# Kernel tuning notes

Hardware: AMD Instinct MI355X
Metric: run time of the kernel (lower is better)

## Reference

```python
import jax, jax.numpy as jnp
import numpy as np

NUM_HEADS = 16


def setup_inputs() -> dict:
    key = jax.random.key(0)
    k1, k2, k3 = jax.random.split(key, 3)
    S, B, E = 2048, 4, 1024
    std = float(np.sqrt(2.0 / (E + E)))
    query = jax.random.normal(k1, (S, B, E), dtype=jnp.float32)
    in_proj_weight = jax.random.normal(k2, (3 * E, E), dtype=jnp.float32) * std
    in_proj_bias = jnp.zeros((3 * E,), dtype=jnp.float32)
    out_proj_weight = jax.random.normal(k3, (E, E), dtype=jnp.float32) * std
    out_proj_bias = jnp.zeros((E,), dtype=jnp.float32)
    return {
        "query": query,
        "in_proj_weight": in_proj_weight,
        "in_proj_bias": in_proj_bias,
        "out_proj_weight": out_proj_weight,
        "out_proj_bias": out_proj_bias,
    }


def reference(query, in_proj_weight, in_proj_bias, out_proj_weight, out_proj_bias):
    S, B, E = query.shape
    H = NUM_HEADS
    hd = E // H
    scale = hd ** -0.5
    # fused QKV projection: [S, B, 3E]
    lin = jnp.einsum("sbe,fe->sbf", query, in_proj_weight) + in_proj_bias
    # torch layout: view(S, B*H, 3, hd) -> interleaved [h, {q,k,v}, hd]
    lin = lin.reshape(S, B * H, 3, hd)
    q = lin[:, :, 0, :]  # [S, B*H, hd]
    k = lin[:, :, 1, :]
    v = lin[:, :, 2, :]
    # scores: [B*H, S_q, S_k]
    scores = jnp.einsum("sbd,tbd->bst", q, k) * scale
    attn = jax.nn.softmax(scores.astype(jnp.float32), axis=-1).astype(scores.dtype)
    # context: [S, B*H, hd] -> [S, B, E]
    ctx = jnp.einsum("bst,tbd->sbd", attn, v).reshape(S, B, E)
    out = jnp.einsum("sbe,fe->sbf", ctx, out_proj_weight) + out_proj_bias
    return out
```

## Files before the change

### kernel.cpp

```cpp
#include <hip/hip_runtime.h>
#include <hip/hip_bf16.h>

typedef __hip_bfloat16 bf16;
typedef __attribute__((ext_vector_type(8))) short short8;
typedef __attribute__((ext_vector_type(4))) float floatx4;

#define GLD_LDS(g, l) __builtin_amdgcn_global_load_lds( \
    (const __attribute__((address_space(1))) void*)(g), \
    (__attribute__((address_space(3))) void*)(l), 16, 0, 0)

#define CS 0.18033688f

__global__ __launch_bounds__(256)
void cvt3_kernel(const float* __restrict__ q,  bf16* __restrict__ qo,
                 const float* __restrict__ w1, bf16* __restrict__ w1o,
                 const float* __restrict__ w2, bf16* __restrict__ w2o)
{
    const int i = blockIdx.x * 256 + threadIdx.x;
    const float* src; bf16* dst; long off;
    if (i < 1048576)       { src = q;  dst = qo;  off = (long)i * 8; }
    else if (i < 1441792)  { src = w1; dst = w1o; off = (long)(i - 1048576) * 8; }
    else                   { src = w2; dst = w2o; off = (long)(i - 1441792) * 8; }
    floatx4 a = *(const floatx4*)(src + off);
    floatx4 b = *(const floatx4*)(src + off + 4);
    short8 h;
    #pragma unroll
    for (int e = 0; e < 4; ++e) {
        union { bf16 v; short s; } u0, u1;
        u0.v = __float2bfloat16(a[e]); h[e]     = u0.s;
        u1.v = __float2bfloat16(b[e]); h[e + 4] = u1.s;
    }
    *(short8*)(dst + off) = h;
}

__device__ __forceinline__ void stage_f32(const float* __restrict__ src, int ld,
                                          bf16* lds, int t)
{
    const int sr = t >> 1;
    const int sc = (t & 1) * 16;
    const float* g = src + (long)sr * ld + sc;
    floatx4 f[4];
    #pragma unroll
    for (int i = 0; i < 4; ++i) f[i] = *(const floatx4*)(g + i * 4);
    short8 h[2];
    #pragma unroll
    for (int v = 0; v < 2; ++v)
        #pragma unroll
        for (int e = 0; e < 8; ++e) {
            union { bf16 b; short s; } u;
            u.b = __float2bfloat16(f[v * 2 + (e >> 2)][e & 3]);
            h[v][e] = u.s;
        }
    *(short8*)(lds + sr * 32 + sc)     = h[0];
    *(short8*)(lds + sr * 32 + sc + 8) = h[1];
}

template<int EPI, int AF32, int BF32>
__global__ __launch_bounds__(256, 2)
void gemm_bt(const void* __restrict__ Ap, const void* __restrict__ Bp,
             const float* __restrict__ bias,
             void* __restrict__ o0, bf16* __restrict__ o1, bf16* __restrict__ o2,
             int K, int N)
{
    __shared__ __align__(16) bf16 lA[128 * 32];
    __shared__ __align__(16) bf16 lB[128 * 32];

    const int t    = threadIdx.x;
    const int lane = t & 63;
    const int w    = t >> 6;
    const int mBase = blockIdx.y * 128;
    const int nBase = blockIdx.x * 128;
    const int wr = (w >> 1) * 64;
    const int wc = (w & 1) * 64;

    const int rowL = t >> 2;
    const int colL = (t & 3) * 8;
    const bf16* gA0 = (const bf16*)Ap + (long)(mBase + rowL) * K + colL;
    const bf16* gA1 = (const bf16*)Ap + (long)(mBase + rowL + 64) * K + colL;
    const bf16* gB0 = (const bf16*)Bp + (long)(nBase + rowL) * K + colL;
    const bf16* gB1 = (const bf16*)Bp + (long)(nBase + rowL + 64) * K + colL;
    char* lAb = (char*)lA + w * 1024;
    char* lBb = (char*)lB + w * 1024;

    floatx4 acc[4][4] = {};

    for (int k0 = 0; k0 < K; k0 += 32) {
        if constexpr (AF32) {
            stage_f32((const float*)Ap + (long)mBase * K + k0, K, lA, t);
        } else {
            GLD_LDS(gA0 + k0, lAb);
            GLD_LDS(gA1 + k0, lAb + 4096);
        }
        if constexpr (BF32) {
            stage_f32((const float*)Bp + (long)nBase * K + k0, K, lB, t);
        } else {
            GLD_LDS(gB0 + k0, lBb);
            GLD_LDS(gB1 + k0, lBb + 4096);
        }
        asm volatile("s_waitcnt vmcnt(0)" ::: "memory");
        __syncthreads();

        short8 af[4], bfr[4];
        #pragma unroll
        for (int m = 0; m < 4; ++m)
            af[m] = *(const short8*)(lA + (wr + m * 16 + (lane & 15)) * 32 + (lane >> 4) * 8);
        #pragma unroll
        for (int n = 0; n < 4; ++n)
            bfr[n] = *(const short8*)(lB + (wc + n * 16 + (lane & 15)) * 32 + (lane >> 4) * 8);
        #pragma unroll
        for (int m = 0; m < 4; ++m)
            #pragma unroll
            for (int n = 0; n < 4; ++n)
                acc[m][n] = __builtin_amdgcn_mfma_f32_16x16x32_bf16(af[m], bfr[n], acc[m][n], 0, 0, 0);
        __syncthreads();
    }

    #pragma unroll
    for (int m = 0; m < 4; ++m) {
        #pragma unroll
        for (int n = 0; n < 4; ++n) {
            const int col = nBase + wc + n * 16 + (lane & 15);
            const int r0  = mBase + wr + m * 16 + ((lane >> 4) << 2);
            const float bv = bias[col];
            if constexpr (EPI == 0) {
                const int h   = col / 192;
                const int rem = col % 192;
                const int qkv = rem >> 6;
                const int d   = rem & 63;
                #pragma unroll
                for (int j = 0; j < 4; ++j) {
                    const int r = r0 + j;
                    const int s = r >> 2;
                    const int b = r & 3;
                    const float v = acc[m][n][j] + bv;
                    if (qkv == 0)
                        ((bf16*)o0)[(((((b << 4) + h) << 11) + s) << 6) + d] =
                            __float2bfloat16(v * CS);
                    else if (qkv == 1)
                        o1[(((((b << 4) + h) << 11) + s) << 6) + d] = __float2bfloat16(v);
                    else
                        o2[((((b << 4) + h) << 17)) + (d << 11) + s] = __float2bfloat16(v);
                }
            } else {
                #pragma unroll
                for (int j = 0; j < 4; ++j)
                    ((float*)o0)[(long)(r0 + j) * N + col] = acc[m][n][j] + bv;
            }
        }
    }
}

__global__ __launch_bounds__(256, 2)
void attn_kernel(const bf16* __restrict__ Q, const bf16* __restrict__ Kg,
                 const bf16* __restrict__ Vt, bf16* __restrict__ Ctx)
{
    __shared__ __align__(16) bf16 lK[64 * 64];
    __shared__ __align__(16) bf16 lV[64 * 64];

    const int t    = threadIdx.x;
    const int lane = t & 63;
    const int w    = t >> 6;
    const int f    = lane & 15;
    const int g    = lane >> 4;
    const int bh   = blockIdx.y;
    const int q0   = blockIdx.x * 128 + w * 32;
    const long hb  = (long)bh * 2048 * 64;
    const bf16* Qh = Q  + hb;
    const bf16* Kh = Kg + hb;
    const bf16* Vh = Vt + hb;

    const int srow = t >> 3;
    const int scol = (t & 7) * 8;
    const int sig0 = (srow & 3) | ((srow & 16) >> 2) | ((srow & 12) << 1);
    const int wb0 = ((srow)      * 128 + scol * 2) ^ (((srow)      & 7) << 4);
    const int wb1 = ((srow + 32) * 128 + scol * 2) ^ (((srow + 32) & 7) << 4);

    short8 qf[2][2];
    #pragma unroll
    for (int m = 0; m < 2; ++m)
        #pragma unroll
        for (int kk = 0; kk < 2; ++kk)
            qf[m][kk] = *(const short8*)(Qh + (q0 + m * 16 + f) * 64 + kk * 32 + g * 8);

    floatx4 o[2][4] = {};
    float lrun[2] = {0.f, 0.f};
    const int srcBase = g * 20;

    short8 kR0 = *(const short8*)(Kh + (long)sig0 * 64 + scol);
    short8 kR1 = *(const short8*)(Kh + (long)(sig0 + 32) * 64 + scol);
    short8 vR0 = *(const short8*)(Vh + (long)srow * 2048 + scol);
    short8 vR1 = *(const short8*)(Vh + (long)(srow + 32) * 2048 + scol);

    for (int t0 = 0; t0 < 2048; t0 += 64) {
        *(short8*)((char*)lK + wb0) = kR0;
        *(short8*)((char*)lK + wb1) = kR1;
        *(short8*)((char*)lV + wb0) = vR0;
        *(short8*)((char*)lV + wb1) = vR1;
        __syncthreads();

        short8 kf[4][2];
        #pragma unroll
        for (int n = 0; n < 4; ++n)
            #pragma unroll
            for (int kk = 0; kk < 2; ++kk) {
                const int key = n * 16 + f;
                const int byte = (key * 128 + kk * 64 + g * 16) ^ ((key & 7) << 4);
                kf[n][kk] = *(const short8*)((char*)lK + byte);
            }

        if (t0 + 64 < 2048) {
            kR0 = *(const short8*)(Kh + (long)(t0 + 64 + sig0) * 64 + scol);
            kR1 = *(const short8*)(Kh + (long)(t0 + 64 + sig0 + 32) * 64 + scol);
            vR0 = *(const short8*)(Vh + (long)srow * 2048 + t0 + 64 + scol);
            vR1 = *(const short8*)(Vh + (long)(srow + 32) * 2048 + t0 + 64 + scol);
        }

        floatx4 sa2[4][2] = {};
        __builtin_amdgcn_s_setprio(1);
        #pragma unroll
        for (int n = 0; n < 4; ++n)
            #pragma unroll
            for (int m = 0; m < 2; ++m)
                #pragma unroll
                for (int kk = 0; kk < 2; ++kk)
                    sa2[n][m] = __builtin_amdgcn_mfma_f32_16x16x32_bf16(kf[n][kk], qf[m][kk], sa2[n][m], 0, 0, 0);
        __builtin_amdgcn_s_setprio(0);

        short8 vf[4][2];
        #pragma unroll
        for (int n2 = 0; n2 < 4; ++n2)
            #pragma unroll
            for (int kk = 0; kk < 2; ++kk) {
                const int dim = n2 * 16 + f;
                const int byte = (dim * 128 + kk * 64 + g * 16) ^ ((dim & 7) << 4);
                vf[n2][kk] = *(const short8*)((char*)lV + byte);
            }

        #pragma unroll
        for (int m = 0; m < 2; ++m)
            #pragma unroll
            for (int n = 0; n < 4; ++n)
                #pragma unroll
                for (int j = 0; j < 4; ++j) {
                    const float p = exp2f(sa2[n][m][j]);
                    sa2[n][m][j] = p;
                    lrun[m] += p;
                }

        short8 pf[2][2];
        #pragma unroll
        for (int m = 0; m < 2; ++m)
            #pragma unroll
            for (int kk = 0; kk < 2; ++kk)
                #pragma unroll
                for (int e = 0; e < 8; ++e) {
                    union { bf16 b; short s; } u;
                    u.b = __float2bfloat16(sa2[2 * kk + (e >> 2)][m][e & 3]);
                    pf[m][kk][e] = u.s;
                }

        __builtin_amdgcn_s_setprio(1);
        #pragma unroll
        for (int m = 0; m < 2; ++m)
            #pragma unroll
            for (int n2 = 0; n2 < 4; ++n2)
                #pragma unroll
                for (int kk = 0; kk < 2; ++kk)
                    o[m][n2] = __builtin_amdgcn_mfma_f32_16x16x32_bf16(pf[m][kk], vf[n2][kk], o[m][n2], 0, 0, 0);
        __builtin_amdgcn_s_setprio(0);

        __syncthreads();
    }

    const int b = bh >> 4;
    const int h = bh & 15;
    #pragma unroll
    for (int m = 0; m < 2; ++m) {
        lrun[m] += __shfl_xor(lrun[m], 16);
        lrun[m] += __shfl_xor(lrun[m], 32);
        float inv[4];
        #pragma unroll
        for (int j = 0; j < 4; ++j)
            inv[j] = 1.f / __shfl(lrun[m], srcBase + j);
        #pragma unroll
        for (int n2 = 0; n2 < 4; ++n2) {
            const int dim = (h << 6) + n2 * 16 + f;
            #pragma unroll
            for (int j = 0; j < 4; ++j) {
                const int srw = q0 + m * 16 + (g << 2) + j;
                Ctx[(((srw << 2) + b) << 10) + dim] = __float2bfloat16(o[m][n2][j] * inv[j]);
            }
        }
    }
}

extern "C" void kernel_launch(void* const* d_in, const int* in_sizes, int n_in,
                              void* d_out, int out_size, void* d_ws, size_t ws_size,
                              hipStream_t stream)
{
    const float* query = (const float*)d_in[0];
    const float* wIn   = (const float*)d_in[1];
    const float* bIn   = (const float*)d_in[2];
    const float* wOut  = (const float*)d_in[3];
    const float* bOut  = (const float*)d_in[4];

    const size_t HEADSZ = (size_t)64 * 2048 * 64;
    bf16* Qws = (bf16*)d_ws;
    bf16* Kws = Qws + HEADSZ;
    bf16* Vtw = Kws + HEADSZ;
    bf16* Ctx = Vtw + HEADSZ;
    bf16* qbf = Ctx;
    if (ws_size < 4 * HEADSZ * sizeof(bf16)) return;

    const size_t NEED_BIG = (4 * HEADSZ + 3145728 + 1048576) * sizeof(bf16);
    if (ws_size >= NEED_BIG) {
        bf16* wInBf  = Ctx + HEADSZ;
        bf16* wOutBf = wInBf + 3145728;
        cvt3_kernel<<<dim3(6144), 256, 0, stream>>>(query, qbf, wIn, wInBf, wOut, wOutBf);
        gemm_bt<0, 0, 0><<<dim3(24, 64), 256, 0, stream>>>(qbf, wInBf, bIn,
                                                           Qws, Kws, Vtw, 1024, 3072);
        attn_kernel<<<dim3(16, 64), 256, 0, stream>>>(Qws, Kws, Vtw, Ctx);
        gemm_bt<1, 0, 0><<<dim3(8, 64), 256, 0, stream>>>(Ctx, wOutBf, bOut,
                                                          d_out, nullptr, nullptr, 1024, 1024);
    } else {
        cvt3_kernel<<<dim3(4096), 256, 0, stream>>>(query, qbf, nullptr, nullptr, nullptr, nullptr);
        gemm_bt<0, 0, 1><<<dim3(24, 64), 256, 0, stream>>>(qbf, wIn, bIn,
                                                           Qws, Kws, Vtw, 1024, 3072);
        attn_kernel<<<dim3(16, 64), 256, 0, stream>>>(Qws, Kws, Vtw, Ctx);
        gemm_bt<1, 0, 1><<<dim3(8, 64), 256, 0, stream>>>(Ctx, wOut, bOut,
                                                          d_out, nullptr, nullptr, 1024, 1024);
    }
}
```

Measured before the change: 224.5 us.

## Double-buffer K/V tiles in LDS and compute softmax denominator via MFMA

Switches the attention kernel to double-buffered LDS for K and V, so the next tile is written into the alternate buffer while the current one is consumed, leaving one barrier per tile instead of two. The row-sum of exponentials is now computed by an extra MFMA against a vector of bf16 ones rather than by scalar adds and cross-lane shuffles. This sums the bf16-rounded probabilities, which matches what is fed to the P·V product. The cost is double the LDS footprint and extra MFMA work per tile.

```diff
diff --git a/kernel.cpp b/kernel.cpp
--- a/kernel.cpp
+++ b/kernel.cpp
@@ -154,8 +154,8 @@
 void attn_kernel(const bf16* __restrict__ Q, const bf16* __restrict__ Kg,
                  const bf16* __restrict__ Vt, bf16* __restrict__ Ctx)
 {
-    __shared__ __align__(16) bf16 lK[64 * 64];
-    __shared__ __align__(16) bf16 lV[64 * 64];
+    __shared__ __align__(16) bf16 lK[2][64 * 64];
+    __shared__ __align__(16) bf16 lV[2][64 * 64];
 
     const int t    = threadIdx.x;
     const int lane = t & 63;
@@ -182,22 +182,29 @@
         for (int kk = 0; kk < 2; ++kk)
             qf[m][kk] = *(const short8*)(Qh + (q0 + m * 16 + f) * 64 + kk * 32 + g * 8);
 
+    short8 ones;
+    #pragma unroll
+    for (int e = 0; e < 8; ++e) ones[e] = (short)0x3F80;
+
     floatx4 o[2][4] = {};
-    float lrun[2] = {0.f, 0.f};
-    const int srcBase = g * 20;
+    floatx4 dn[2] = {};
 
     short8 kR0 = *(const short8*)(Kh + (long)sig0 * 64 + scol);
     short8 kR1 = *(const short8*)(Kh + (long)(sig0 + 32) * 64 + scol);
     short8 vR0 = *(const short8*)(Vh + (long)srow * 2048 + scol);
     short8 vR1 = *(const short8*)(Vh + (long)(srow + 32) * 2048 + scol);
-
-    for (int t0 = 0; t0 < 2048; t0 += 64) {
-        *(short8*)((char*)lK + wb0) = kR0;
-        *(short8*)((char*)lK + wb1) = kR1;
-        *(short8*)((char*)lV + wb0) = vR0;
-        *(short8*)((char*)lV + wb1) = vR1;
-        __syncthreads();
-
+    *(short8*)((char*)lK[0] + wb0) = kR0;
+    *(short8*)((char*)lK[0] + wb1) = kR1;
+    *(short8*)((char*)lV[0] + wb0) = vR0;
+    *(short8*)((char*)lV[0] + wb1) = vR1;
+    kR0 = *(const short8*)(Kh + (long)(64 + sig0) * 64 + scol);
+    kR1 = *(const short8*)(Kh + (long)(64 + sig0 + 32) * 64 + scol);
+    vR0 = *(const short8*)(Vh + (long)srow * 2048 + 64 + scol);
+    vR1 = *(const short8*)(Vh + (long)(srow + 32) * 2048 + 64 + scol);
+    __syncthreads();
+
+    auto tile = [&](const bf16* curK, const bf16* curV,
+                    bf16* nxtK, bf16* nxtV, int t0) __attribute__((always_inline)) {
         short8 kf[4][2];
         #pragma unroll
         for (int n = 0; n < 4; ++n)
@@ -205,14 +212,20 @@
             for (int kk = 0; kk < 2; ++kk) {
                 const int key = n * 16 + f;
                 const int byte = (key * 128 + kk * 64 + g * 16) ^ ((key & 7) << 4);
-                kf[n][kk] = *(const short8*)((char*)lK + byte);
+                kf[n][kk] = *(const short8*)((const char*)curK + byte);
             }
 
         if (t0 + 64 < 2048) {
-            kR0 = *(const short8*)(Kh + (long)(t0 + 64 + sig0) * 64 + scol);
-            kR1 = *(const short8*)(Kh + (long)(t0 + 64 + sig0 + 32) * 64 + scol);
-            vR0 = *(const short8*)(Vh + (long)srow * 2048 + t0 + 64 + scol);
-            vR1 = *(const short8*)(Vh + (long)(srow + 32) * 2048 + t0 + 64 + scol);
+            *(short8*)((char*)nxtK + wb0) = kR0;
+            *(short8*)((char*)nxtK + wb1) = kR1;
+            *(short8*)((char*)nxtV + wb0) = vR0;
+            *(short8*)((char*)nxtV + wb1) = vR1;
+        }
+        if (t0 + 128 < 2048) {
+            kR0 = *(const short8*)(Kh + (long)(t0 + 128 + sig0) * 64 + scol);
+            kR1 = *(const short8*)(Kh + (long)(t0 + 128 + sig0 + 32) * 64 + scol);
+            vR0 = *(const short8*)(Vh + (long)srow * 2048 + t0 + 128 + scol);
+            vR1 = *(const short8*)(Vh + (long)(srow + 32) * 2048 + t0 + 128 + scol);
         }
 
         floatx4 sa2[4][2] = {};
@@ -233,19 +246,8 @@
             for (int kk = 0; kk < 2; ++kk) {
                 const int dim = n2 * 16 + f;
                 const int byte = (dim * 128 + kk * 64 + g * 16) ^ ((dim & 7) << 4);
-                vf[n2][kk] = *(const short8*)((char*)lV + byte);
+                vf[n2][kk] = *(const short8*)((const char*)curV + byte);
             }
-
-        #pragma unroll
-        for (int m = 0; m < 2; ++m)
-            #pragma unroll
-            for (int n = 0; n < 4; ++n)
-                #pragma unroll
-                for (int j = 0; j < 4; ++j) {
-                    const float p = exp2f(sa2[n][m][j]);
-                    sa2[n][m][j] = p;
-                    lrun[m] += p;
-                }
 
         short8 pf[2][2];
         #pragma unroll
@@ -255,33 +257,40 @@
                 #pragma unroll
                 for (int e = 0; e < 8; ++e) {
                     union { bf16 b; short s; } u;
-                    u.b = __float2bfloat16(sa2[2 * kk + (e >> 2)][m][e & 3]);
+                    u.b = __float2bfloat16(exp2f(sa2[2 * kk + (e >> 2)][m][e & 3]));
                     pf[m][kk][e] = u.s;
                 }
 
         __builtin_amdgcn_s_setprio(1);
         #pragma unroll
-        for (int m = 0; m < 2; ++m)
+        for (int m = 0; m < 2; ++m) {
             #pragma unroll
             for (int n2 = 0; n2 < 4; ++n2)
                 #pragma unroll
                 for (int kk = 0; kk < 2; ++kk)
                     o[m][n2] = __builtin_amdgcn_mfma_f32_16x16x32_bf16(pf[m][kk], vf[n2][kk], o[m][n2], 0, 0, 0);
+            #pragma unroll
+            for (int kk = 0; kk < 2; ++kk)
+                dn[m] = __builtin_amdgcn_mfma_f32_16x16x32_bf16(pf[m][kk], ones, dn[m], 0, 0, 0);
+        }
         __builtin_amdgcn_s_setprio(0);
 
         __syncthreads();
+    };
+
+    for (int t0 = 0; t0 < 2048; t0 += 128) {
+        tile(lK[0], lV[0], lK[1], lV[1], t0);
+        tile(lK[1], lV[1], lK[0], lV[0], t0 + 64);
     }
 
     const int b = bh >> 4;
     const int h = bh & 15;
     #pragma unroll
     for (int m = 0; m < 2; ++m) {
-        lrun[m] += __shfl_xor(lrun[m], 16);
-        lrun[m] += __shfl_xor(lrun[m], 32);
         float inv[4];
         #pragma unroll
         for (int j = 0; j < 4; ++j)
-            inv[j] = 1.f / __shfl(lrun[m], srcBase + j);
+            inv[j] = 1.f / dn[m][j];
         #pragma unroll
         for (int n2 = 0; n2 < 4; ++n2) {
             const int dim = (h << 6) + n2 * 16 + f;
```

Result: no change. 221.1 us (-1.5%).
